# Kernel optimization log

Hardware: AMD Instinct MI355X
Metric: run time of the kernel (lower is better)

## Reference

```python
import jax, jax.numpy as jnp
import numpy as np

N_NODES = 50000
N_EDGES = 800000


def graph_conv(h, W, b, src, dst, n_nodes):
    # DGL GraphConv with norm='both':
    #   out = D_in^{-1/2} * A^T * (D_out^{-1/2} * h) @ W + b
    ones = jnp.ones((src.shape[0],), dtype=h.dtype)
    deg_out = jax.ops.segment_sum(ones, src, num_segments=n_nodes)
    deg_in = jax.ops.segment_sum(ones, dst, num_segments=n_nodes)
    norm_src = jnp.clip(deg_out, 1.0) ** -0.5  # [N]
    norm_dst = jnp.clip(deg_in, 1.0) ** -0.5   # [N]
    msg = (h * norm_src[:, None])[src]          # [E, F] gather
    agg = jax.ops.segment_sum(msg, dst, num_segments=n_nodes)  # [N, F] scatter
    return (agg * norm_dst[:, None]) @ W + b


def setup_inputs() -> dict:
    key = jax.random.key(0)
    ks = jax.random.split(key, 5)
    h = jax.random.normal(ks[0], (N_NODES, 64), dtype=jnp.float32)
    src = jax.random.randint(ks[1], (N_EDGES,), 0, N_NODES, dtype=jnp.int32)
    dst = jax.random.randint(ks[2], (N_EDGES,), 0, N_NODES, dtype=jnp.int32)
    W1 = jax.random.normal(ks[3], (64, 128), dtype=jnp.float32) * (1.0 / np.sqrt(64))
    b1 = jnp.zeros((128,), dtype=jnp.float32)
    W2 = jax.random.normal(ks[4], (128, 64), dtype=jnp.float32) * (1.0 / np.sqrt(128))
    b2 = jnp.zeros((64,), dtype=jnp.float32)
    return {"h": h, "src": src, "dst": dst, "W1": W1, "b1": b1, "W2": W2, "b2": b2}


def reference(h, src, dst, W1, b1, W2, b2):
    n = h.shape[0]
    h1 = jax.nn.relu(graph_conv(h, W1, b1, src, dst, n))
    out = graph_conv(h1, W2, b2, src, dst, n)
    return out
```

## Files before the change

### kernel.cpp

```cpp
#include <hip/hip_runtime.h>


#define NBMAX 512
#define CAPLOG 12
#define CAP (1 << CAPLOG)

__device__ inline unsigned short f2bf(float f) {
    unsigned int u = __float_as_uint(f);
    unsigned int r = (u + 0x7FFFu + ((u >> 16) & 1u)) >> 16;
    return (unsigned short)r;
}
__device__ inline float bf2f_lo(unsigned int u) { return __uint_as_float(u << 16); }
__device__ inline float bf2f_hi(unsigned int u) { return __uint_as_float(u & 0xFFFF0000u); }
__device__ inline float bf2f(unsigned short h) {
    return __uint_as_float((unsigned int)h << 16);
}

__global__ __launch_bounds__(256) void place_direct(const int* __restrict__ src,
        const int* __restrict__ dst, int* __restrict__ cnt_s, int* __restrict__ cnt_d,
        unsigned char* __restrict__ ss, unsigned int* __restrict__ sd,
        int n_edges, int nb) {
    __shared__ int hs[NBMAX], hd[NBMAX], bs[NBMAX], bd[NBMAX];
    for (int i = threadIdx.x; i < nb; i += 256) { hs[i] = 0; hd[i] = 0; }
    __syncthreads();
    int chunk = (n_edges + gridDim.x - 1) / gridDim.x;
    int e0 = blockIdx.x * chunk;
    int e1 = e0 + chunk; if (e1 > n_edges) e1 = n_edges;
    for (int e = e0 + (int)threadIdx.x; e < e1; e += 256) {
        atomicAdd(&hs[src[e] >> 7], 1);
        atomicAdd(&hd[dst[e] >> 7], 1);
    }
    __syncthreads();
    for (int i = threadIdx.x; i < nb; i += 256) {
        int v = hs[i]; bs[i] = v ? atomicAdd(&cnt_s[i], v) : 0; hs[i] = 0;
        v = hd[i];     bd[i] = v ? atomicAdd(&cnt_d[i], v) : 0; hd[i] = 0;
    }
    __syncthreads();
    for (int e = e0 + (int)threadIdx.x; e < e1; e += 256) {
        int s = src[e], d = dst[e];
        int sb = s >> 7, db = d >> 7;
        int ps = bs[sb] + atomicAdd(&hs[sb], 1);
        ss[((size_t)sb << CAPLOG) + ps] = (unsigned char)(s & 127);
        int pd = bd[db] + atomicAdd(&hd[db], 1);
        sd[((size_t)db << CAPLOG) + pd] = ((unsigned int)(d & 127) << 25) | (unsigned int)s;
    }
}

__global__ __launch_bounds__(256) void prep(const float* __restrict__ h,
        const unsigned char* __restrict__ ss, const int* __restrict__ cnt_s,
        const unsigned int* __restrict__ sd, const int* __restrict__ cnt_d,
        float* __restrict__ norm_src, unsigned short* __restrict__ xb,
        int2* __restrict__ node_rng, unsigned short* __restrict__ srt,
        float* __restrict__ norm_dst, int n) {
    __shared__ int cnt[128], cur[128];
    __shared__ float nrm[128];
    __shared__ int w0tot;
    const int b = blockIdx.x;
    const int tid = threadIdx.x;

    if (tid < 128) cnt[tid] = 0;
    __syncthreads();
    {
        int used = cnt_s[b];
        const unsigned char* p = ss + ((size_t)b << CAPLOG);
        for (int i = tid; i < used; i += 256) atomicAdd(&cnt[p[i]], 1);
    }
    __syncthreads();
    if (tid < 128) {
        int c = cnt[tid]; if (c < 1) c = 1;
        float s = 1.0f / sqrtf((float)c);
        nrm[tid] = s;
        int node = (b << 7) + tid;
        if (node < n) norm_src[node] = s;
    }
    __syncthreads();
    {
        int base = b << 7;
        for (int t = tid; t < 128 * 16; t += 256) {
            int r = t >> 4, c4 = (t & 15) << 2;
            int node = base + r;
            if (node < n) {
                float s = nrm[r];
                float4 v = *(const float4*)(h + (size_t)node * 64 + c4);
                ushort4 o;
                o.x = f2bf(v.x * s); o.y = f2bf(v.y * s);
                o.z = f2bf(v.z * s); o.w = f2bf(v.w * s);
                *(ushort4*)(xb + (size_t)node * 64 + c4) = o;
            }
        }
    }
    __syncthreads();

    if (tid < 128) cnt[tid] = 0;
    __syncthreads();
    int used = cnt_d[b];
    const unsigned int* p = sd + ((size_t)b << CAPLOG);
    for (int i = tid; i < used; i += 256) atomicAdd(&cnt[p[i] >> 25], 1);
    __syncthreads();
    int lane = tid & 63, wid = tid >> 6;
    int v = (tid < 128) ? cnt[tid] : 0;
    int incl = v;
    #pragma unroll
    for (int d = 1; d < 64; d <<= 1) {
        int t = __shfl_up(incl, d, 64);
        if (lane >= d) incl += t;
    }
    if (tid == 63) w0tot = incl;
    __syncthreads();
    if (tid < 128) {
        int excl = incl - v + (wid == 1 ? w0tot : 0);
        cur[tid] = excl;
        int node = (b << 7) + tid;
        if (node < n) {
            int base = b << CAPLOG;
            node_rng[node] = make_int2(base + excl, base + excl + v);
            int c = v; if (c < 1) c = 1;
            norm_dst[node] = 1.0f / sqrtf((float)c);
        }
    }
    __syncthreads();
    for (int i = tid; i < used; i += 256) {
        unsigned int e = p[i];
        int l = (int)(e >> 25);
        int pos = atomicAdd(&cur[l], 1);
        srt[((size_t)b << CAPLOG) + pos] = (unsigned short)(e & 0xFFFFu);
    }
}

__global__ __launch_bounds__(256) void gather24(const unsigned short* __restrict__ xb,
        const unsigned short* __restrict__ srt, const int2* __restrict__ node_rng,
        const float* __restrict__ nrm, const float* __restrict__ bias,
        void* __restrict__ outp, int write_bf, int n_nodes) {
    int node = blockIdx.x * 4 + (threadIdx.x >> 6);
    if (node >= n_nodes) return;
    int lane = threadIdx.x & 63;
    int g  = lane >> 3;
    int c8 = (lane & 7) * 8;
    int2 rng = node_rng[node];
    int a0 = rng.x, a1 = rng.y;
    float acc[8];
    #pragma unroll
    for (int j = 0; j < 8; ++j) acc[j] = 0.f;
    for (int base = a0; base < a1; base += 24) {
        #pragma unroll
        for (int u = 0; u < 3; ++u) {
            int ei = base + u * 8 + g;
            int idx = ei < a1 ? ei : a1 - 1;
            float msk = ei < a1 ? 1.0f : 0.0f;
            int s = srt[idx];
            const uint4 v = *(const uint4*)(xb + (size_t)s * 64 + c8);
            acc[0] = fmaf(bf2f_lo(v.x), msk, acc[0]);
            acc[1] = fmaf(bf2f_hi(v.x), msk, acc[1]);
            acc[2] = fmaf(bf2f_lo(v.y), msk, acc[2]);
            acc[3] = fmaf(bf2f_hi(v.y), msk, acc[3]);
            acc[4] = fmaf(bf2f_lo(v.z), msk, acc[4]);
            acc[5] = fmaf(bf2f_hi(v.z), msk, acc[5]);
            acc[6] = fmaf(bf2f_lo(v.w), msk, acc[6]);
            acc[7] = fmaf(bf2f_hi(v.w), msk, acc[7]);
        }
    }
    #pragma unroll
    for (int off = 8; off < 64; off <<= 1) {
        #pragma unroll
        for (int j = 0; j < 8; ++j) acc[j] += __shfl_xor(acc[j], off, 64);
    }
    if (g == 0) {
        float s = nrm[node];
        float r[8];
        #pragma unroll
        for (int j = 0; j < 8; ++j) r[j] = acc[j] * s;
        if (write_bf) {
            unsigned short rb[8];
            #pragma unroll
            for (int j = 0; j < 8; ++j) rb[j] = f2bf(r[j]);
            unsigned short* o = (unsigned short*)outp + (size_t)node * 64 + c8;
            *(ushort4*)(o)     = make_ushort4(rb[0], rb[1], rb[2], rb[3]);
            *(ushort4*)(o + 4) = make_ushort4(rb[4], rb[5], rb[6], rb[7]);
        } else {
            if (bias) {
                #pragma unroll
                for (int j = 0; j < 8; ++j) r[j] += bias[c8 + j];
            }
            float* o = (float*)outp + (size_t)node * 64 + c8;
            *(float4*)(o)     = make_float4(r[0], r[1], r[2], r[3]);
            *(float4*)(o + 4) = make_float4(r[4], r[5], r[6], r[7]);
        }
    }
}

__global__ __launch_bounds__(256) void gemm1(const unsigned short* __restrict__ Ab,
        const float* __restrict__ W1, const float* __restrict__ b1,
        const float* __restrict__ norm, unsigned short* __restrict__ H1b, int n_nodes) {
    __shared__ float Ws[64 * 128];
    __shared__ float As[64 * 68];
    __shared__ float b1s[128];
    const int tid = threadIdx.x;
    for (int idx = tid; idx < 64 * 128; idx += 256) Ws[idx] = W1[idx];
    if (tid < 128) b1s[tid] = b1[tid];

    const int m0 = blockIdx.x * 64;
    const ushort4* Ag = (const ushort4*)(Ab + (size_t)m0 * 64);
    #pragma unroll
    for (int i = 0; i < 4; ++i) {
        int idx = tid + i * 256;
        int m = idx >> 4;
        int k4 = (idx & 15) * 4;
        float4 v = make_float4(0.f, 0.f, 0.f, 0.f);
        if (m0 + m < n_nodes) {
            ushort4 u = Ag[idx];
            v.x = bf2f(u.x); v.y = bf2f(u.y); v.z = bf2f(u.z); v.w = bf2f(u.w);
        }
        *(float4*)(As + m * 68 + k4) = v;
    }
    __syncthreads();

    const int tx = tid & 15;
    const int ty = tid >> 4;
    float acc[4][8];
    #pragma unroll
    for (int i = 0; i < 4; ++i)
        #pragma unroll
        for (int j = 0; j < 8; ++j) acc[i][j] = 0.0f;

    const float* Ap = As + ty * 4 * 68;
    const float* Wp = Ws + tx * 8;
    for (int k = 0; k < 64; ++k) {
        float a0 = Ap[k];
        float a1 = Ap[68 + k];
        float a2 = Ap[136 + k];
        float a3 = Ap[204 + k];
        float w[8];
        #pragma unroll
        for (int j = 0; j < 8; ++j) w[j] = Wp[k * 128 + j];
        #pragma unroll
        for (int j = 0; j < 8; ++j) {
            acc[0][j] = fmaf(a0, w[j], acc[0][j]);
            acc[1][j] = fmaf(a1, w[j], acc[1][j]);
            acc[2][j] = fmaf(a2, w[j], acc[2][j]);
            acc[3][j] = fmaf(a3, w[j], acc[3][j]);
        }
    }

    #pragma unroll
    for (int i = 0; i < 4; ++i) {
        int node = m0 + ty * 4 + i;
        if (node < n_nodes) {
            float s = norm[node];
            unsigned short r[8];
            #pragma unroll
            for (int j = 0; j < 8; ++j) {
                float v = acc[i][j] + b1s[tx * 8 + j];
                v = v > 0.0f ? v : 0.0f;
                r[j] = f2bf(v * s);
            }
            unsigned short* o = H1b + (size_t)node * 128 + tx * 8;
            *(ushort4*)(o)     = make_ushort4(r[0], r[1], r[2], r[3]);
            *(ushort4*)(o + 4) = make_ushort4(r[4], r[5], r[6], r[7]);
        }
    }
}

__global__ __launch_bounds__(256) void gemm2b(const unsigned short* __restrict__ H1b,
        const float* __restrict__ W2, unsigned short* __restrict__ y2b, int n_nodes) {
    __shared__ float Ws[128 * 64];
    __shared__ float Hs[64 * 132];
    const int tid = threadIdx.x;
    for (int idx = tid; idx < 128 * 64; idx += 256) Ws[idx] = W2[idx];

    const int m0 = blockIdx.x * 64;
    const ushort4* Hg = (const ushort4*)(H1b + (size_t)m0 * 128);
    #pragma unroll
    for (int i = 0; i < 8; ++i) {
        int idx = tid + i * 256;
        int m = idx >> 5;
        int k4 = (idx & 31) * 4;
        float4 v = make_float4(0.f, 0.f, 0.f, 0.f);
        if (m0 + m < n_nodes) {
            ushort4 u = Hg[idx];
            v.x = bf2f(u.x); v.y = bf2f(u.y); v.z = bf2f(u.z); v.w = bf2f(u.w);
        }
        *(float4*)(Hs + m * 132 + k4) = v;
    }
    __syncthreads();

    const int tx = tid & 15;
    const int ty = tid >> 4;
    float acc[4][4];
    #pragma unroll
    for (int i = 0; i < 4; ++i)
        #pragma unroll
        for (int j = 0; j < 4; ++j) acc[i][j] = 0.0f;

    const float* Ap = Hs + ty * 4 * 132;
    for (int k = 0; k < 128; ++k) {
        float a0 = Ap[k];
        float a1 = Ap[132 + k];
        float a2 = Ap[264 + k];
        float a3 = Ap[396 + k];
        const float4 w = *(const float4*)(Ws + k * 64 + tx * 4);
        acc[0][0] = fmaf(a0, w.x, acc[0][0]); acc[0][1] = fmaf(a0, w.y, acc[0][1]);
        acc[0][2] = fmaf(a0, w.z, acc[0][2]); acc[0][3] = fmaf(a0, w.w, acc[0][3]);
        acc[1][0] = fmaf(a1, w.x, acc[1][0]); acc[1][1] = fmaf(a1, w.y, acc[1][1]);
        acc[1][2] = fmaf(a1, w.z, acc[1][2]); acc[1][3] = fmaf(a1, w.w, acc[1][3]);
        acc[2][0] = fmaf(a2, w.x, acc[2][0]); acc[2][1] = fmaf(a2, w.y, acc[2][1]);
        acc[2][2] = fmaf(a2, w.z, acc[2][2]); acc[2][3] = fmaf(a2, w.w, acc[2][3]);
        acc[3][0] = fmaf(a3, w.x, acc[3][0]); acc[3][1] = fmaf(a3, w.y, acc[3][1]);
        acc[3][2] = fmaf(a3, w.z, acc[3][2]); acc[3][3] = fmaf(a3, w.w, acc[3][3]);
    }

    #pragma unroll
    for (int i = 0; i < 4; ++i) {
        int node = m0 + ty * 4 + i;
        if (node < n_nodes) {
            ushort4 o;
            o.x = f2bf(acc[i][0]); o.y = f2bf(acc[i][1]);
            o.z = f2bf(acc[i][2]); o.w = f2bf(acc[i][3]);
            *(ushort4*)(y2b + (size_t)node * 64 + tx * 4) = o;
        }
    }
}

extern "C" void kernel_launch(void* const* d_in, const int* in_sizes, int n_in,
                              void* d_out, int out_size, void* d_ws, size_t ws_size,
                              hipStream_t stream) {
    const float* h   = (const float*)d_in[0];
    const int*   src = (const int*)d_in[1];
    const int*   dst = (const int*)d_in[2];
    const float* W1  = (const float*)d_in[3];
    const float* b1  = (const float*)d_in[4];
    const float* W2  = (const float*)d_in[5];
    const float* b2  = (const float*)d_in[6];
    float* out = (float*)d_out;

    const int n = in_sizes[0] / 64;
    const int E = in_sizes[1];
    const int nb = (n + 127) >> 7;

    char* p = (char*)d_ws;
    auto alloc = [&](size_t bytes) {
        void* r = (void*)p;
        p += (bytes + 255) & ~(size_t)255;
        return r;
    };
    float* norm_src      = (float*)alloc((size_t)n * 4);
    float* norm_dst      = (float*)alloc((size_t)n * 4);
    int2* node_rng       = (int2*)alloc((size_t)n * 8);
    int* cnt2            = (int*)alloc((size_t)2 * nb * 4);
    int* cnt_s = cnt2;
    int* cnt_d = cnt2 + nb;
    unsigned int* sd     = (unsigned int*)alloc((size_t)nb * CAP * 4);
    unsigned short* xb   = (unsigned short*)alloc((size_t)n * 64 * 2);
    unsigned short* agg1b= (unsigned short*)alloc((size_t)n * 64 * 2);
    unsigned short* H1b  = (unsigned short*)alloc((size_t)n * 128 * 2);
    unsigned short* y2b  = (unsigned short*)alloc((size_t)n * 64 * 2);
    unsigned short* srt  = (unsigned short*)alloc((size_t)nb * CAP * 2);
    unsigned char* ssb   = (unsigned char*)alloc((size_t)nb * CAP);

    hipMemsetAsync(cnt2, 0, 2 * (size_t)nb * sizeof(int), stream);

    place_direct<<<256, 256, 0, stream>>>(src, dst, cnt_s, cnt_d, ssb, sd, E, nb);
    prep<<<nb, 256, 0, stream>>>(h, ssb, cnt_s, sd, cnt_d, norm_src, xb,
                                 node_rng, srt, norm_dst, n);

    int gb = (n + 3) / 4;
    gather24<<<gb, 256, 0, stream>>>(xb, srt, node_rng, norm_dst, nullptr,
                                     (void*)agg1b, 1, n);

    int tb = (n + 63) / 64;
    gemm1<<<tb, 256, 0, stream>>>(agg1b, W1, b1, norm_src, H1b, n);
    gemm2b<<<tb, 256, 0, stream>>>(H1b, W2, y2b, n);

    gather24<<<gb, 256, 0, stream>>>(y2b, srt, node_rng, norm_dst, b2,
                                     (void*)out, 0, n);
}
```

Baseline: 195.8 us.

## Fuse the two dense GEMMs into one kernel with bf16 shared-memory tiles

Merges gemm1 and gemm2b into a single kernel. The 64x128 hidden tile stays in shared memory, so the H1 intermediate no longer makes a round trip through global memory and one launch is removed. Weights and activations are now held in shared memory as bf16 instead of fp32, which cuts LDS footprint and allows wider packed loads. In exchange, each block converts both weight matrices to bf16 on entry, which is redundant per-block work and adds rounding on the weights.

```diff
diff --git a/kernel.cpp b/kernel.cpp
--- a/kernel.cpp
+++ b/kernel.cpp
@@ -188,133 +188,121 @@
     }
 }
 
-__global__ __launch_bounds__(256) void gemm1(const unsigned short* __restrict__ Ab,
+__global__ __launch_bounds__(256) void gemm12(const unsigned short* __restrict__ Ab,
         const float* __restrict__ W1, const float* __restrict__ b1,
-        const float* __restrict__ norm, unsigned short* __restrict__ H1b, int n_nodes) {
-    __shared__ float Ws[64 * 128];
-    __shared__ float As[64 * 68];
+        const float* __restrict__ norm, const float* __restrict__ W2,
+        unsigned short* __restrict__ y2b, int n_nodes) {
+    __shared__ unsigned short W1b[64 * 128];
+    __shared__ unsigned short W2b[128 * 64];
+    __shared__ unsigned short As[64 * 74];
+    __shared__ unsigned short Hs[64 * 138];
     __shared__ float b1s[128];
     const int tid = threadIdx.x;
-    for (int idx = tid; idx < 64 * 128; idx += 256) Ws[idx] = W1[idx];
+    for (int i = tid; i < 8192; i += 256) W1b[i] = f2bf(W1[i]);
+    for (int i = tid; i < 8192; i += 256) W2b[i] = f2bf(W2[i]);
     if (tid < 128) b1s[tid] = b1[tid];
 
     const int m0 = blockIdx.x * 64;
     const ushort4* Ag = (const ushort4*)(Ab + (size_t)m0 * 64);
-    #pragma unroll
-    for (int i = 0; i < 4; ++i) {
-        int idx = tid + i * 256;
-        int m = idx >> 4;
-        int k4 = (idx & 15) * 4;
-        float4 v = make_float4(0.f, 0.f, 0.f, 0.f);
-        if (m0 + m < n_nodes) {
-            ushort4 u = Ag[idx];
-            v.x = bf2f(u.x); v.y = bf2f(u.y); v.z = bf2f(u.z); v.w = bf2f(u.w);
-        }
-        *(float4*)(As + m * 68 + k4) = v;
+    for (int i = tid; i < 1024; i += 256) {
+        int m = i >> 4, k4 = (i & 15) << 2;
+        ushort4 u = make_ushort4(0, 0, 0, 0);
+        if (m0 + m < n_nodes) u = Ag[i];
+        *(ushort4*)(As + m * 74 + k4) = u;
     }
     __syncthreads();
 
     const int tx = tid & 15;
     const int ty = tid >> 4;
+
     float acc[4][8];
     #pragma unroll
     for (int i = 0; i < 4; ++i)
         #pragma unroll
-        for (int j = 0; j < 8; ++j) acc[i][j] = 0.0f;
-
-    const float* Ap = As + ty * 4 * 68;
-    const float* Wp = Ws + tx * 8;
-    for (int k = 0; k < 64; ++k) {
-        float a0 = Ap[k];
-        float a1 = Ap[68 + k];
-        float a2 = Ap[136 + k];
-        float a3 = Ap[204 + k];
-        float w[8];
-        #pragma unroll
-        for (int j = 0; j < 8; ++j) w[j] = Wp[k * 128 + j];
-        #pragma unroll
-        for (int j = 0; j < 8; ++j) {
-            acc[0][j] = fmaf(a0, w[j], acc[0][j]);
-            acc[1][j] = fmaf(a1, w[j], acc[1][j]);
-            acc[2][j] = fmaf(a2, w[j], acc[2][j]);
-            acc[3][j] = fmaf(a3, w[j], acc[3][j]);
-        }
-    }
-
+        for (int j = 0; j < 8; ++j) acc[i][j] = 0.f;
+    {
+        const unsigned short* Ap = As + ty * 4 * 74;
+        const unsigned short* Wp = W1b + tx * 8;
+        for (int k = 0; k < 64; k += 4) {
+            uint2 ar[4];
+            #pragma unroll
+            for (int i = 0; i < 4; ++i) ar[i] = *(const uint2*)(Ap + i * 74 + k);
+            #pragma unroll
+            for (int kk = 0; kk < 4; ++kk) {
+                const uint4 wv = *(const uint4*)(Wp + (k + kk) * 128);
+                float w0 = bf2f_lo(wv.x), w1 = bf2f_hi(wv.x);
+                float w2 = bf2f_lo(wv.y), w3 = bf2f_hi(wv.y);
+                float w4 = bf2f_lo(wv.z), w5 = bf2f_hi(wv.z);
+                float w6 = bf2f_lo(wv.w), w7 = bf2f_hi(wv.w);
+                #pragma unroll
+                for (int i = 0; i < 4; ++i) {
+                    unsigned int half = (kk < 2) ? ar[i].x : ar[i].y;
+                    float a = (kk & 1) ? bf2f_hi(half) : bf2f_lo(half);
+                    acc[i][0] = fmaf(a, w0, acc[i][0]);
+                    acc[i][1] = fmaf(a, w1, acc[i][1]);
+                    acc[i][2] = fmaf(a, w2, acc[i][2]);
+                    acc[i][3] = fmaf(a, w3, acc[i][3]);
+                    acc[i][4] = fmaf(a, w4, acc[i][4]);
+                    acc[i][5] = fmaf(a, w5, acc[i][5]);
+                    acc[i][6] = fmaf(a, w6, acc[i][6]);
+                    acc[i][7] = fmaf(a, w7, acc[i][7]);
+                }
+            }
+        }
+    }
     #pragma unroll
     for (int i = 0; i < 4; ++i) {
         int node = m0 + ty * 4 + i;
-        if (node < n_nodes) {
-            float s = norm[node];
-            unsigned short r[8];
-            #pragma unroll
-            for (int j = 0; j < 8; ++j) {
-                float v = acc[i][j] + b1s[tx * 8 + j];
-                v = v > 0.0f ? v : 0.0f;
-                r[j] = f2bf(v * s);
+        float s = (node < n_nodes) ? norm[node] : 0.f;
+        unsigned short r[8];
+        #pragma unroll
+        for (int j = 0; j < 8; ++j) {
+            float v = acc[i][j] + b1s[tx * 8 + j];
+            v = v > 0.f ? v : 0.f;
+            r[j] = f2bf(v * s);
+        }
+        unsigned short* o = Hs + (ty * 4 + i) * 138 + tx * 8;
+        *(ushort4*)(o)     = make_ushort4(r[0], r[1], r[2], r[3]);
+        *(ushort4*)(o + 4) = make_ushort4(r[4], r[5], r[6], r[7]);
+    }
+    __syncthreads();
+
+    float ac2[4][4];
+    #pragma unroll
+    for (int i = 0; i < 4; ++i)
+        #pragma unroll
+        for (int j = 0; j < 4; ++j) ac2[i][j] = 0.f;
+    {
+        const unsigned short* Hp = Hs + ty * 4 * 138;
+        const unsigned short* Wp = W2b + tx * 4;
+        for (int k = 0; k < 128; k += 4) {
+            uint2 hr[4];
+            #pragma unroll
+            for (int i = 0; i < 4; ++i) hr[i] = *(const uint2*)(Hp + i * 138 + k);
+            #pragma unroll
+            for (int kk = 0; kk < 4; ++kk) {
+                const uint2 wv = *(const uint2*)(Wp + (k + kk) * 64);
+                float w0 = bf2f_lo(wv.x), w1 = bf2f_hi(wv.x);
+                float w2 = bf2f_lo(wv.y), w3 = bf2f_hi(wv.y);
+                #pragma unroll
+                for (int i = 0; i < 4; ++i) {
+                    unsigned int half = (kk < 2) ? hr[i].x : hr[i].y;
+                    float a = (kk & 1) ? bf2f_hi(half) : bf2f_lo(half);
+                    ac2[i][0] = fmaf(a, w0, ac2[i][0]);
+                    ac2[i][1] = fmaf(a, w1, ac2[i][1]);
+                    ac2[i][2] = fmaf(a, w2, ac2[i][2]);
+                    ac2[i][3] = fmaf(a, w3, ac2[i][3]);
+                }
             }
-            unsigned short* o = H1b + (size_t)node * 128 + tx * 8;
-            *(ushort4*)(o)     = make_ushort4(r[0], r[1], r[2], r[3]);
-            *(ushort4*)(o + 4) = make_ushort4(r[4], r[5], r[6], r[7]);
-        }
-    }
-}
-
-__global__ __launch_bounds__(256) void gemm2b(const unsigned short* __restrict__ H1b,
-        const float* __restrict__ W2, unsigned short* __restrict__ y2b, int n_nodes) {
-    __shared__ float Ws[128 * 64];
-    __shared__ float Hs[64 * 132];
-    const int tid = threadIdx.x;
-    for (int idx = tid; idx < 128 * 64; idx += 256) Ws[idx] = W2[idx];
-
-    const int m0 = blockIdx.x * 64;
-    const ushort4* Hg = (const ushort4*)(H1b + (size_t)m0 * 128);
-    #pragma unroll
-    for (int i = 0; i < 8; ++i) {
-        int idx = tid + i * 256;
-        int m = idx >> 5;
-        int k4 = (idx & 31) * 4;
-        float4 v = make_float4(0.f, 0.f, 0.f, 0.f);
-        if (m0 + m < n_nodes) {
-            ushort4 u = Hg[idx];
-            v.x = bf2f(u.x); v.y = bf2f(u.y); v.z = bf2f(u.z); v.w = bf2f(u.w);
-        }
-        *(float4*)(Hs + m * 132 + k4) = v;
-    }
-    __syncthreads();
-
-    const int tx = tid & 15;
-    const int ty = tid >> 4;
-    float acc[4][4];
-    #pragma unroll
-    for (int i = 0; i < 4; ++i)
-        #pragma unroll
-        for (int j = 0; j < 4; ++j) acc[i][j] = 0.0f;
-
-    const float* Ap = Hs + ty * 4 * 132;
-    for (int k = 0; k < 128; ++k) {
-        float a0 = Ap[k];
-        float a1 = Ap[132 + k];
-        float a2 = Ap[264 + k];
-        float a3 = Ap[396 + k];
-        const float4 w = *(const float4*)(Ws + k * 64 + tx * 4);
-        acc[0][0] = fmaf(a0, w.x, acc[0][0]); acc[0][1] = fmaf(a0, w.y, acc[0][1]);
-        acc[0][2] = fmaf(a0, w.z, acc[0][2]); acc[0][3] = fmaf(a0, w.w, acc[0][3]);
-        acc[1][0] = fmaf(a1, w.x, acc[1][0]); acc[1][1] = fmaf(a1, w.y, acc[1][1]);
-        acc[1][2] = fmaf(a1, w.z, acc[1][2]); acc[1][3] = fmaf(a1, w.w, acc[1][3]);
-        acc[2][0] = fmaf(a2, w.x, acc[2][0]); acc[2][1] = fmaf(a2, w.y, acc[2][1]);
-        acc[2][2] = fmaf(a2, w.z, acc[2][2]); acc[2][3] = fmaf(a2, w.w, acc[2][3]);
-        acc[3][0] = fmaf(a3, w.x, acc[3][0]); acc[3][1] = fmaf(a3, w.y, acc[3][1]);
-        acc[3][2] = fmaf(a3, w.z, acc[3][2]); acc[3][3] = fmaf(a3, w.w, acc[3][3]);
-    }
-
+        }
+    }
     #pragma unroll
     for (int i = 0; i < 4; ++i) {
         int node = m0 + ty * 4 + i;
         if (node < n_nodes) {
             ushort4 o;
-            o.x = f2bf(acc[i][0]); o.y = f2bf(acc[i][1]);
-            o.z = f2bf(acc[i][2]); o.w = f2bf(acc[i][3]);
+            o.x = f2bf(ac2[i][0]); o.y = f2bf(ac2[i][1]);
+            o.z = f2bf(ac2[i][2]); o.w = f2bf(ac2[i][3]);
             *(ushort4*)(y2b + (size_t)node * 64 + tx * 4) = o;
         }
     }
@@ -351,7 +339,6 @@
     unsigned int* sd     = (unsigned int*)alloc((size_t)nb * CAP * 4);
     unsigned short* xb   = (unsigned short*)alloc((size_t)n * 64 * 2);
     unsigned short* agg1b= (unsigned short*)alloc((size_t)n * 64 * 2);
-    unsigned short* H1b  = (unsigned short*)alloc((size_t)n * 128 * 2);
     unsigned short* y2b  = (unsigned short*)alloc((size_t)n * 64 * 2);
     unsigned short* srt  = (unsigned short*)alloc((size_t)nb * CAP * 2);
     unsigned char* ssb   = (unsigned char*)alloc((size_t)nb * CAP);
@@ -367,8 +354,7 @@
                                      (void*)agg1b, 1, n);
 
     int tb = (n + 63) / 64;
-    gemm1<<<tb, 256, 0, stream>>>(agg1b, W1, b1, norm_src, H1b, n);
-    gemm2b<<<tb, 256, 0, stream>>>(H1b, W2, y2b, n);
+    gemm12<<<tb, 256, 0, stream>>>(agg1b, W1, b1, norm_src, W2, y2b, n);
 
     gather24<<<gb, 256, 0, stream>>>(y2b, srt, node_rng, norm_dst, b2,
                                      (void*)out, 0, n);
```

Measured after the change: 218.1 us. 11.4% more time.
